# Optimization experiments

Hardware: AMD Instinct MI355X
Metric: run time of the kernel (lower is better)

Reference implementation:

```python
import math
import jax
import jax.numpy as jnp
from jax import lax
import numpy as np

B, T, S, C, E = 16, 1024, 2048, 256, 256
STRIDE, MAX_SAMPLES, SIGMA, RAND_START = 20, 20, 3.0, 0


def setup_inputs():
    key = jax.random.key(0)
    ks = jax.random.split(key, 6)
    return {
        "x": jax.random.normal(ks[0], (B, T, C), jnp.float32),
        "target_embedding": jax.random.normal(ks[1], (B, T, E), jnp.float32),
        # scale keys so pre-softmax scores are O(1..10) like a trained model
        "enc_keys": jax.random.normal(ks[2], (B, E, S), jnp.float32) * 0.05,
        "enc_values": jax.random.normal(ks[3], (B, S, E), jnp.float32),
        "W_in": jax.random.normal(ks[4], (E, C), jnp.float32) * math.sqrt(1.0 / C),
        "b_in": jnp.zeros((E,), jnp.float32),
        "W_out": jax.random.normal(ks[5], (C, E), jnp.float32) * math.sqrt(1.0 / E),
        "b_out": jnp.zeros((C,), jnp.float32),
    }


def _get_matrix(attn, sim_vec, stride, start):
    # attn: [B,T,S], sim_vec: [B,S,E]
    nrm = sim_vec / jnp.linalg.norm(sim_vec, axis=2, keepdims=True)
    attn_avg = jnp.mean(attn, axis=1)[..., None]          # [B,S,1]
    ns = nrm[:, start::stride, :]                          # [B,N,E]
    aa = attn_avg[:, start::stride, :]                     # [B,N,1]
    sim = jnp.einsum('bne,bme->bnm', ns, ns)               # cosine similarity
    qual = aa @ jnp.swapaxes(aa, 1, 2)                     # quality outer product
    return qual * sim                                      # DPP kernel L [B,N,N]


def _bfgm(L, max_samples):
    # Vectorized faithful version of the greedy Cholesky DPP MAP loop.
    Bv, N, _ = L.shape
    bidx = jnp.arange(Bv)
    D0 = jnp.diagonal(L, axis1=1, axis2=2)                 # [B,N]
    mask0 = jnp.ones((Bv, N), L.dtype)
    J0 = jnp.argmax(jnp.log(D0 * mask0), axis=1)
    mask0 = mask0.at[bidx, J0].set(0.0)
    C0 = jnp.zeros((Bv, N, max_samples), L.dtype)          # col 0 stays zero (as in torch)

    def step(carry, t):
        Cm, D, J, mask = carry
        Lj = L[bidx, J, :]                                 # [B,N] = L[b, J[b], i]
        cj = Cm[bidx, J, :]                                # [B,K]
        cdot = jnp.einsum('bnk,bk->bn', Cm, cj)            # <c_i, c_j>
        dj = D[bidx, J][:, None]
        e = (Lj - cdot) / dj * mask                        # zero at already-selected
        Cm = Cm.at[:, :, t].set(e)
        D = D - e * e
        J = jnp.argmax(jnp.log(D * mask), axis=1)
        mask = mask.at[bidx, J].set(0.0)
        return (Cm, D, J, mask), J

    (_, _, _, _), Js = lax.scan(step, (C0, D0, J0, mask0), jnp.arange(1, max_samples))
    all_J = jnp.concatenate([J0[None, :], Js], axis=0).T   # [B,max_samples]
    return jnp.sort(all_J, axis=1)                         # = nonzero(1-mask) order


def _create_gm(mu, sigma, length):
    pos = jnp.arange(length, dtype=jnp.float32)            # [S]
    z = pos[None, None, :] - mu[:, :, None].astype(jnp.float32)
    g = jnp.exp(-(z * z) / (2.0 * sigma * sigma)) / (math.sqrt(2.0 * math.pi) * sigma)
    return jnp.sum(g, axis=1)                              # [B,S]


def _forward(x, target_embedding, enc_keys, enc_values, W_in, b_in, W_out, b_out):
    residual = x
    h = (jnp.einsum('btc,ec->bte', x, W_in) + b_in + target_embedding) * math.sqrt(0.5)
    scores = jnp.einsum('bte,bes->bts', h, enc_keys)       # [B,T,S]
    attn = jax.nn.softmax(scores, axis=-1)
    # DPP auxiliary KL loss (training path, encoder_padding_mask=None); the
    # kernel / greedy selection / target distribution carry no gradient.
    L = _get_matrix(lax.stop_gradient(attn), lax.stop_gradient(enc_values), STRIDE, RAND_START)
    mu = _bfgm(L, MAX_SAMPLES)
    dist = jax.nn.softmax(_create_gm(mu, SIGMA, scores.shape[2]), axis=1)
    x_mean = jnp.mean(attn, axis=1)                        # [B,S]
    kl = jnp.sum(x_mean * (jnp.log(x_mean) - dist))        # KLDivLoss(input=dist, target=x_mean, sum)
    out = jnp.einsum('bts,bse->bte', attn, enc_values)
    s = enc_values.shape[1]
    out = out * (s * math.sqrt(1.0 / s))                   # = sqrt(s)
    out = (jnp.einsum('bte,ce->btc', out, W_out) + b_out + residual) * math.sqrt(0.5)
    return out, attn, -kl


def reference(x, target_embedding, enc_keys, enc_values, W_in, b_in, W_out, b_out):
    return _forward(x, target_embedding, enc_keys, enc_values, W_in, b_in, W_out, b_out)
```

## Files before the change

### kernel.cpp

```cpp
#include <hip/hip_runtime.h>
#include <math.h>

#define BB 16
#define TT 1024
#define SS 2048
#define CC 256
#define EE 256
#define NSUB 103
#define MAXS 20
#define STRIDE_ 20
#define XCH 32

static constexpr float RSQRT2  = 0.70710678118654752440f;
static constexpr float SQRT_S  = 45.25483399593904f;
static constexpr float GNORM   = 0.13298076013381093f;
static constexpr float INV2S2  = 0.055555555555555555f;

typedef __attribute__((ext_vector_type(8))) __bf16 bf16x8;
typedef __attribute__((ext_vector_type(4))) float  f32x4;

__device__ __forceinline__ float wave_sum(float v) {
    #pragma unroll
    for (int o = 32; o; o >>= 1) v += __shfl_down(v, o);
    return v;
}
__device__ __forceinline__ float wave_max(float v) {
    #pragma unroll
    for (int o = 32; o; o >>= 1) v = fmaxf(v, __shfl_down(v, o));
    return v;
}
__device__ __forceinline__ unsigned short f2bf(float f) {
    unsigned int u = __float_as_uint(f);
    u = (u + 0x7FFFu + ((u >> 16) & 1u)) >> 16;
    return (unsigned short)u;
}
__device__ __forceinline__ float bf2f(unsigned short s) {
    return __uint_as_float(((unsigned int)s) << 16);
}

#define GLD_LDS16(g, l) __builtin_amdgcn_global_load_lds(                      \
    (const __attribute__((address_space(1))) void*)(g),                        \
    (__attribute__((address_space(3))) void*)(l), 16, 0, 0)

__global__ __launch_bounds__(256) void k_cast3(
    const float* __restrict__ a,  unsigned short* __restrict__ oa, int na,
    const float* __restrict__ b2, unsigned short* __restrict__ ob, int nb,
    const float* __restrict__ c2, unsigned short* __restrict__ oc, int nc)
{
    int i = blockIdx.x * 256 + threadIdx.x;
    const float* in; unsigned short* out;
    if (i < na)                { in = a;  out = oa; }
    else if (i < na + nb)      { in = b2; out = ob; i -= na; }
    else if (i < na + nb + nc) { in = c2; out = oc; i -= na + nb; }
    else return;
    const float4 v = reinterpret_cast<const float4*>(in)[i];
    union { unsigned short u[4]; unsigned long long v8; } pk;
    pk.u[0] = f2bf(v.x); pk.u[1] = f2bf(v.y);
    pk.u[2] = f2bf(v.z); pk.u[3] = f2bf(v.w);
    reinterpret_cast<unsigned long long*>(out)[i] = pk.v8;
}

__global__ __launch_bounds__(256) void k_transpose2(
    const float* __restrict__ keys, unsigned short* __restrict__ keysT,
    const float* __restrict__ vals, unsigned short* __restrict__ valsT)
{
    __shared__ float t[64][65];
    const int id = blockIdx.x;
    const float* in; unsigned short* out;
    int R, Cc, bx, by, b;
    if (id < 2048) {
        in = keys; out = keysT; R = EE; Cc = SS;
        bx = id & 3; by = (id >> 2) & 31; b = id >> 7;
    } else {
        const int id2 = id - 2048;
        in = vals; out = valsT; R = SS; Cc = EE;
        bx = id2 & 31; by = (id2 >> 5) & 3; b = id2 >> 7;
    }
    const int r0 = bx * 64, c0 = by * 64;
    const float* ip = in + (size_t)b * R * Cc;
    unsigned short* op = out + (size_t)b * R * Cc;
    const int tx = threadIdx.x & 63, ty = threadIdx.x >> 6;
    #pragma unroll
    for (int i = 0; i < 16; ++i)
        t[ty + 4 * i][tx] = ip[(size_t)(r0 + ty + 4 * i) * Cc + c0 + tx];
    __syncthreads();
    #pragma unroll
    for (int i = 0; i < 16; ++i)
        op[(size_t)(c0 + ty + 4 * i) * R + r0 + tx] = f2bf(t[tx][ty + 4 * i]);
}

template<int BM, int BN, int MODE>
__global__ __launch_bounds__(256) void k_gemm(
    const unsigned short* __restrict__ Abase,
    const unsigned short* __restrict__ Btbase,
    const float* __restrict__ bias, const float* __restrict__ add,
    float* __restrict__ Obase, unsigned short* __restrict__ Obbase,
    int M, int Nn, int K, float scale)
{
    constexpr int BK = 64;
    constexpr int AR = BM / 32;
    constexpr int BR = BN / 32;
    constexpr int WM = BM / 2, WN = BN / 2;
    constexpr int MI = WM / 16, NJ = WN / 16;

    __shared__ unsigned short As[BM * BK];
    __shared__ unsigned short Bs[BN * BK];

    const int nwg = gridDim.x * gridDim.y * gridDim.z;
    int l = blockIdx.x + gridDim.x * (blockIdx.y + gridDim.y * blockIdx.z);
    if ((nwg & 7) == 0) l = (l & 7) * (nwg >> 3) + (l >> 3);
    const int bx = l % gridDim.x; l /= gridDim.x;
    const int by = l % gridDim.y;
    const int b  = l / gridDim.y;

    const int m0 = bx * BM;
    const int n0 = by * BN;
    const unsigned short* A  = Abase  + (size_t)b * M  * K;
    const unsigned short* Bt = Btbase + (size_t)b * Nn * K;

    const int tid  = threadIdx.x;
    const int w    = tid >> 6;
    const int lane = tid & 63;
    const int wm   = w & 1, wn = w >> 1;

    const int sr  = tid >> 3;
    const int skb = ((tid & 7) << 4) ^ ((sr & 7) << 4);
    const unsigned short* ga[AR];
    const unsigned short* gb[BR];
    #pragma unroll
    for (int p = 0; p < AR; ++p)
        ga[p] = A + (size_t)(m0 + p * 32 + sr) * K + (skb >> 1);
    #pragma unroll
    for (int p = 0; p < BR; ++p)
        gb[p] = Bt + (size_t)(n0 + p * 32 + sr) * K + (skb >> 1);

    const int fr = lane & 15;
    const int qb = (lane >> 4) << 4;

    f32x4 acc[MI][NJ];
    #pragma unroll
    for (int i = 0; i < MI; ++i)
        #pragma unroll
        for (int j = 0; j < NJ; ++j)
            acc[i][j] = (f32x4){0.f, 0.f, 0.f, 0.f};

    for (int k0 = 0; k0 < K; k0 += BK) {
        #pragma unroll
        for (int p = 0; p < AR; ++p) GLD_LDS16(ga[p], As + p * 2048 + w * 512);
        #pragma unroll
        for (int p = 0; p < BR; ++p) GLD_LDS16(gb[p], Bs + p * 2048 + w * 512);
        #pragma unroll
        for (int p = 0; p < AR; ++p) ga[p] += BK;
        #pragma unroll
        for (int p = 0; p < BR; ++p) gb[p] += BK;
        __syncthreads();
        #pragma unroll
        for (int c = 0; c < 2; ++c) {
            bf16x8 af[MI], bf[NJ];
            #pragma unroll
            for (int i = 0; i < MI; ++i) {
                const int row = wm * WM + i * 16 + fr;
                const int byt = row * 128 + ((c * 64 + qb) ^ ((row & 7) << 4));
                af[i] = *reinterpret_cast<const bf16x8*>(
                            reinterpret_cast<const char*>(As) + byt);
            }
            #pragma unroll
            for (int j = 0; j < NJ; ++j) {
                const int row = wn * WN + j * 16 + fr;
                const int byt = row * 128 + ((c * 64 + qb) ^ ((row & 7) << 4));
                bf[j] = *reinterpret_cast<const bf16x8*>(
                            reinterpret_cast<const char*>(Bs) + byt);
            }
            #pragma unroll
            for (int i = 0; i < MI; ++i)
                #pragma unroll
                for (int j = 0; j < NJ; ++j)
                    acc[i][j] = __builtin_amdgcn_mfma_f32_16x16x32_bf16(af[i], bf[j], acc[i][j], 0, 0, 0);
        }
        __syncthreads();
    }

    float* Of = (MODE == 0 || MODE == 1) ? Obase + (size_t)b * M * Nn : nullptr;
    unsigned short* Ob = (MODE == 2 || MODE == 3) ? Obbase + (size_t)b * M * Nn : nullptr;
    const int rb = (lane >> 4) * 4;
    #pragma unroll
    for (int i = 0; i < MI; ++i)
        #pragma unroll
        for (int j = 0; j < NJ; ++j) {
            const int n = n0 + wn * WN + j * 16 + fr;
            #pragma unroll
            for (int r2 = 0; r2 < 4; ++r2) {
                const int m = m0 + wm * WM + i * 16 + rb + r2;
                const size_t idx = (size_t)m * Nn + n;
                if (MODE == 0) {
                    Of[idx] = acc[i][j][r2] * scale;
                } else if (MODE == 1) {
                    Of[idx] = (acc[i][j][r2] + bias[n] + add[idx]) * RSQRT2;
                } else if (MODE == 2) {
                    Ob[idx] = f2bf((acc[i][j][r2] + bias[n] + add[idx]) * RSQRT2);
                } else {
                    Ob[idx] = f2bf(acc[i][j][r2] * scale);
                }
            }
        }
}

__global__ __launch_bounds__(256) void k_softmax(float* __restrict__ attn,
                                                 unsigned short* __restrict__ attnb)
{
    const int row  = blockIdx.x * 4 + (threadIdx.x >> 6);
    const int lane = threadIdx.x & 63;
    float* p = attn + (size_t)row * SS;
    unsigned short* pb = attnb + (size_t)row * SS;

    float v[32];
    #pragma unroll
    for (int s = 0; s < 4; ++s) {
        union { unsigned short u[8]; uint4 q; } ld;
        ld.q = *reinterpret_cast<const uint4*>(&pb[s * 512 + lane * 8]);
        #pragma unroll
        for (int i = 0; i < 8; ++i) v[s * 8 + i] = bf2f(ld.u[i]);
    }
    float mx = v[0];
    #pragma unroll
    for (int i = 1; i < 32; ++i) mx = fmaxf(mx, v[i]);
    #pragma unroll
    for (int o = 32; o; o >>= 1) mx = fmaxf(mx, __shfl_xor(mx, o));
    float s = 0.f;
    #pragma unroll
    for (int i = 0; i < 32; ++i) { v[i] = expf(v[i] - mx); s += v[i]; }
    #pragma unroll
    for (int o = 32; o; o >>= 1) s += __shfl_xor(s, o);
    const float inv = 1.0f / s;
    #pragma unroll
    for (int seg = 0; seg < 4; ++seg) {
        float4 o0, o1;
        o0.x = v[seg * 8 + 0] * inv; o0.y = v[seg * 8 + 1] * inv;
        o0.z = v[seg * 8 + 2] * inv; o0.w = v[seg * 8 + 3] * inv;
        o1.x = v[seg * 8 + 4] * inv; o1.y = v[seg * 8 + 5] * inv;
        o1.z = v[seg * 8 + 6] * inv; o1.w = v[seg * 8 + 7] * inv;
        *reinterpret_cast<float4*>(&p[seg * 512 + lane * 8])     = o0;
        *reinterpret_cast<float4*>(&p[seg * 512 + lane * 8 + 4]) = o1;
        union { unsigned short u[8]; uint4 q; } pk;
        pk.u[0] = f2bf(o0.x); pk.u[1] = f2bf(o0.y); pk.u[2] = f2bf(o0.z); pk.u[3] = f2bf(o0.w);
        pk.u[4] = f2bf(o1.x); pk.u[5] = f2bf(o1.y); pk.u[6] = f2bf(o1.z); pk.u[7] = f2bf(o1.w);
        *reinterpret_cast<uint4*>(&pb[seg * 512 + lane * 8]) = pk.q;
    }
}

__global__ __launch_bounds__(256) void k_xmean_part(const unsigned short* __restrict__ attnb,
                                                    float* __restrict__ part)
{
    const int c = blockIdx.x, b = blockIdx.y;
    const unsigned short* p = attnb + ((size_t)b * TT + (size_t)c * (TT / XCH)) * SS
                              + threadIdx.x * 8;
    float acc[8] = {0.f, 0.f, 0.f, 0.f, 0.f, 0.f, 0.f, 0.f};
    #pragma unroll 8
    for (int t = 0; t < TT / XCH; ++t) {
        union { unsigned short u[8]; uint4 v4; } ld;
        ld.v4 = *reinterpret_cast<const uint4*>(p + (size_t)t * SS);
        #pragma unroll
        for (int i = 0; i < 8; ++i) acc[i] += bf2f(ld.u[i]);
    }
    float* o = part + ((size_t)b * XCH + c) * SS + threadIdx.x * 8;
    #pragma unroll
    for (int i = 0; i < 8; ++i) o[i] = acc[i];
}

__global__ __launch_bounds__(256) void k_ns(const float* __restrict__ ev,
                                            const float* __restrict__ part,
                                            float* __restrict__ ns, float* __restrict__ aa,
                                            float* __restrict__ klp)
{
    const int n = blockIdx.x, b = blockIdx.y;
    const int tid = threadIdx.x;
    if (n == 0 && b == 0 && tid == 0) klp[0] = 0.0f;
    const float* rowp = ev + ((size_t)b * SS + (size_t)n * STRIDE_) * EE;
    const float v = rowp[tid];
    __shared__ float w[4];
    float r = wave_sum(v * v);
    if ((tid & 63) == 0) w[tid >> 6] = r;
    float pv = (tid < XCH) ? part[((size_t)b * XCH + tid) * SS + n * STRIDE_] : 0.f;
    float psum = wave_sum(pv);
    __syncthreads();
    const float nrm = sqrtf(w[0] + w[1] + w[2] + w[3]);
    ns[((size_t)b * NSUB + n) * EE + tid] = v / nrm;
    if (tid == 0) aa[b * NSUB + n] = psum * (1.0f / TT);
}

__global__ __launch_bounds__(128) void k_L(const float* __restrict__ ns,
                                           const float* __restrict__ aa,
                                           float* __restrict__ Lm)
{
    const int i = blockIdx.x, b = blockIdx.y;
    const int tid = threadIdx.x;
    __shared__ float nsi[EE];
    nsi[tid]       = ns[((size_t)b * NSUB + i) * EE + tid];
    nsi[tid + 128] = ns[((size_t)b * NSUB + i) * EE + tid + 128];
    __syncthreads();
    const float ai = aa[b * NSUB + i];
    for (int j = tid; j < NSUB; j += 128) {
        const float* rj = ns + ((size_t)b * NSUB + j) * EE;
        float d = 0.f;
        #pragma unroll 4
        for (int e = 0; e < EE; ++e) d += nsi[e] * rj[e];
        Lm[((size_t)b * NSUB + i) * NSUB + j] = d * ai * aa[b * NSUB + j];
    }
}

__global__ __launch_bounds__(256) void k_bfgm_kl(const float* __restrict__ Lm,
                                                 const float* __restrict__ part,
                                                 float* __restrict__ outkl)
{
    const int b = blockIdx.x;
    const int tid = threadIdx.x;
    const float* L = Lm + (size_t)b * NSUB * NSUB;
    __shared__ float D[128], mask[128], Cm[128 * 21], cj[MAXS], musS[MAXS];
    __shared__ float rv[4];
    __shared__ int   ri[4];
    __shared__ int   Jsh;
    __shared__ float w[4];
    const bool half = tid < 128;
    const bool act  = tid < NSUB;
    if (half) {
        D[tid]    = act ? L[(size_t)tid * NSUB + tid] : 0.0f;
        mask[tid] = act ? 1.0f : 0.0f;
        #pragma unroll
        for (int k = 0; k < MAXS; ++k) Cm[tid * 21 + k] = 0.0f;
    }
    __syncthreads();

    auto argmax_step = [&](int t) {
        float key = act ? logf(D[tid] * mask[tid]) : -INFINITY;
        if (isnan(key)) key = INFINITY;
        float v = key; int idx = tid;
        #pragma unroll
        for (int o = 32; o; o >>= 1) {
            float ov = __shfl_down(v, o); int oi = __shfl_down(idx, o);
            if (ov > v || (ov == v && oi < idx)) { v = ov; idx = oi; }
        }
        if ((tid & 63) == 0) { rv[tid >> 6] = v; ri[tid >> 6] = idx; }
        __syncthreads();
        if (tid == 0) {
            float bv = rv[0]; int bi = ri[0];
            #pragma unroll
            for (int q2 = 1; q2 < 4; ++q2)
                if (rv[q2] > bv || (rv[q2] == bv && ri[q2] < bi)) { bv = rv[q2]; bi = ri[q2]; }
            Jsh = bi; mask[bi] = 0.0f; musS[t] = (float)bi;
        }
        __syncthreads();
    };

    argmax_step(0);
    for (int t = 1; t < MAXS; ++t) {
        if (tid < MAXS) cj[tid] = Cm[Jsh * 21 + tid];
        __syncthreads();
        const int J = Jsh;
        const float dj = D[J];
        float e = 0.0f;
        if (act) {
            const float Ljn = L[(size_t)J * NSUB + tid];
            float cd = 0.f;
            #pragma unroll
            for (int k = 0; k < MAXS; ++k) cd += Cm[tid * 21 + k] * cj[k];
            e = (Ljn - cd) / dj * mask[tid];
        }
        if (half) { Cm[tid * 21 + t] = e; D[tid] -= e * e; }
        __syncthreads();
        argmax_step(t);
    }

    float xm[8];
    #pragma unroll
    for (int i = 0; i < 8; ++i) {
        float s = 0.f;
        #pragma unroll 8
        for (int c2 = 0; c2 < XCH; ++c2)
            s += part[((size_t)b * XCH + c2) * SS + tid + (i << 8)];
        xm[i] = s * (1.0f / TT);
    }
    float g[8];
    float mx = -INFINITY;
    #pragma unroll
    for (int i = 0; i < 8; ++i) {
        const float s = (float)(tid + (i << 8));
        float acc = 0.f;
        #pragma unroll
        for (int m = 0; m < MAXS; ++m) { const float z = s - musS[m]; acc += expf(-(z * z) * INV2S2); }
        g[i] = acc * GNORM;
        mx = fmaxf(mx, g[i]);
    }
    float wm = wave_max(mx);
    if ((tid & 63) == 0) w[tid >> 6] = wm;
    __syncthreads();
    const float m = fmaxf(fmaxf(w[0], w[1]), fmaxf(w[2], w[3]));
    float sum = 0.f;
    #pragma unroll
    for (int i = 0; i < 8; ++i) { g[i] = expf(g[i] - m); sum += g[i]; }
    __syncthreads();
    float wsv = wave_sum(sum);
    if ((tid & 63) == 0) w[tid >> 6] = wsv;
    __syncthreads();
    const float inv = 1.0f / (w[0] + w[1] + w[2] + w[3]);
    float acc2 = 0.f;
    #pragma unroll
    for (int i = 0; i < 8; ++i)
        acc2 += xm[i] * (logf(xm[i]) - g[i] * inv);
    __syncthreads();
    float wp = wave_sum(acc2);
    if ((tid & 63) == 0) w[tid >> 6] = wp;
    __syncthreads();
    if (tid == 0) atomicAdd(outkl, -(w[0] + w[1] + w[2] + w[3]));
}

extern "C" void kernel_launch(void* const* d_in, const int* in_sizes, int n_in,
                              void* d_out, int out_size, void* d_ws, size_t ws_size,
                              hipStream_t stream)
{
    const float* x     = (const float*)d_in[0];
    const float* te    = (const float*)d_in[1];
    const float* keys  = (const float*)d_in[2];
    const float* vals  = (const float*)d_in[3];
    const float* W_in  = (const float*)d_in[4];
    const float* b_in  = (const float*)d_in[5];
    const float* W_out = (const float*)d_in[6];
    const float* b_out = (const float*)d_in[7];

    float* outp = (float*)d_out;
    float* attn = outp + (size_t)BB * TT * CC;
    float* klp  = attn + (size_t)BB * TT * SS;

    unsigned short* X       = (unsigned short*)d_ws;
    unsigned short* x_bf    = X;
    unsigned short* Win_bf  = x_bf   + (size_t)BB * TT * CC;
    unsigned short* Wout_bf = Win_bf + (size_t)EE * CC;
    unsigned short* h_bf    = Wout_bf+ (size_t)CC * EE;
    unsigned short* keysT   = h_bf   + (size_t)BB * TT * EE;
    unsigned short* valsT   = keysT  + (size_t)BB * SS * EE;
    unsigned short* attnb   = valsT  + (size_t)BB * EE * SS;
    unsigned short* mid_bf  = attnb  + (size_t)BB * TT * SS;
    float* fws   = (float*)(mid_bf + (size_t)BB * TT * EE + 8);
    float* part  = fws;
    float* ns    = part  + (size_t)BB * XCH * SS;
    float* aa    = ns    + (size_t)BB * NSUB * EE;
    float* Lm    = aa    + (size_t)BB * NSUB;

    {
        const int na = BB * TT * CC / 4, nb = EE * CC / 4, nc = CC * EE / 4;
        const int blocks = (na + nb + nc + 255) / 256;
        k_cast3<<<blocks, 256, 0, stream>>>(x, x_bf, na, W_in, Win_bf, nb, W_out, Wout_bf, nc);
    }
    k_gemm<64, 64, 2><<<dim3(256, 4, 1), 256, 0, stream>>>(
        x_bf, Win_bf, b_in, te, nullptr, h_bf, BB * TT, CC, CC, 1.0f);
    k_transpose2<<<4096, 256, 0, stream>>>(keys, keysT, vals, valsT);
    k_gemm<128, 128, 3><<<dim3(8, 16, BB), 256, 0, stream>>>(
        h_bf, keysT, nullptr, nullptr, nullptr, attnb, TT, SS, EE, 1.0f);
    k_softmax<<<BB * TT / 4, 256, 0, stream>>>(attn, attnb);
    k_xmean_part<<<dim3(XCH, BB), 256, 0, stream>>>(attnb, part);
    k_ns<<<dim3(NSUB, BB), 256, 0, stream>>>(vals, part, ns, aa, klp);
    k_L<<<dim3(NSUB, BB), 128, 0, stream>>>(ns, aa, Lm);
    k_bfgm_kl<<<BB, 256, 0, stream>>>(Lm, part, klp);
    k_gemm<64, 128, 3><<<dim3(16, 2, BB), 256, 0, stream>>>(
        attnb, valsT, nullptr, nullptr, nullptr, mid_bf, TT, EE, SS, SQRT_S);
    k_gemm<64, 64, 1><<<dim3(256, 4, 1), 256, 0, stream>>>(
        mid_bf, Wout_bf, b_out, x, outp, nullptr, BB * TT, CC, CC, 1.0f);
}
```

Measured before the change: 460.1 us.

## Fuse normalization into L kernel and run greedy DPP loop in one wave

Removes the separate k_ns kernel by computing row norms and attention averages inside the L-matrix kernel, which reads enc_values rows directly with float4 loads. The greedy Cholesky DPP selection is rewritten to run within a single 64-lane wave, two items per lane, using shuffles for the argmax instead of block-wide syncthreads. The goal is to cut one launch and the many barriers in the sequential 20-step loop. In exchange, each j row's norm is recomputed redundantly across blocks, and correctness now depends on single-wave LDS visibility through __threadfence_block.

```diff
diff --git a/kernel.cpp b/kernel.cpp
--- a/kernel.cpp
+++ b/kernel.cpp
@@ -249,9 +249,11 @@
 }
 
 __global__ __launch_bounds__(256) void k_xmean_part(const unsigned short* __restrict__ attnb,
-                                                    float* __restrict__ part)
+                                                    float* __restrict__ part,
+                                                    float* __restrict__ klp)
 {
     const int c = blockIdx.x, b = blockIdx.y;
+    if (c == 0 && b == 0 && threadIdx.x == 0) klp[0] = 0.0f;
     const unsigned short* p = attnb + ((size_t)b * TT + (size_t)c * (TT / XCH)) * SS
                               + threadIdx.x * 8;
     float acc[8] = {0.f, 0.f, 0.f, 0.f, 0.f, 0.f, 0.f, 0.f};
@@ -267,44 +269,41 @@
     for (int i = 0; i < 8; ++i) o[i] = acc[i];
 }
 
-__global__ __launch_bounds__(256) void k_ns(const float* __restrict__ ev,
-                                            const float* __restrict__ part,
-                                            float* __restrict__ ns, float* __restrict__ aa,
-                                            float* __restrict__ klp)
-{
-    const int n = blockIdx.x, b = blockIdx.y;
-    const int tid = threadIdx.x;
-    if (n == 0 && b == 0 && tid == 0) klp[0] = 0.0f;
-    const float* rowp = ev + ((size_t)b * SS + (size_t)n * STRIDE_) * EE;
-    const float v = rowp[tid];
-    __shared__ float w[4];
-    float r = wave_sum(v * v);
-    if ((tid & 63) == 0) w[tid >> 6] = r;
-    float pv = (tid < XCH) ? part[((size_t)b * XCH + tid) * SS + n * STRIDE_] : 0.f;
-    float psum = wave_sum(pv);
-    __syncthreads();
-    const float nrm = sqrtf(w[0] + w[1] + w[2] + w[3]);
-    ns[((size_t)b * NSUB + n) * EE + tid] = v / nrm;
-    if (tid == 0) aa[b * NSUB + n] = psum * (1.0f / TT);
-}
-
-__global__ __launch_bounds__(128) void k_L(const float* __restrict__ ns,
-                                           const float* __restrict__ aa,
-                                           float* __restrict__ Lm)
+__global__ __launch_bounds__(128) void k_L_direct(const float* __restrict__ ev,
+                                                  const float* __restrict__ part,
+                                                  float* __restrict__ Lm)
 {
     const int i = blockIdx.x, b = blockIdx.y;
     const int tid = threadIdx.x;
-    __shared__ float nsi[EE];
-    nsi[tid]       = ns[((size_t)b * NSUB + i) * EE + tid];
-    nsi[tid + 128] = ns[((size_t)b * NSUB + i) * EE + tid + 128];
-    __syncthreads();
-    const float ai = aa[b * NSUB + i];
+    __shared__ float evi[EE];
+    __shared__ float aaS[NSUB];
+    __shared__ float w[2];
+    const float* rowi = ev + ((size_t)b * SS + (size_t)i * STRIDE_) * EE;
+    const float v0 = rowi[tid], v1 = rowi[tid + 128];
+    evi[tid] = v0; evi[tid + 128] = v1;
+    const float r = wave_sum(v0 * v0 + v1 * v1);
+    if ((tid & 63) == 0) w[tid >> 6] = r;
+    if (tid < NSUB) {
+        float s = 0.f;
+        #pragma unroll 8
+        for (int c2 = 0; c2 < XCH; ++c2)
+            s += part[((size_t)b * XCH + c2) * SS + tid * STRIDE_];
+        aaS[tid] = s * (1.0f / TT);
+    }
+    __syncthreads();
+    const float nrmi = sqrtf(w[0] + w[1]);
+    const float ai = aaS[i];
     for (int j = tid; j < NSUB; j += 128) {
-        const float* rj = ns + ((size_t)b * NSUB + j) * EE;
-        float d = 0.f;
+        const float* rj = ev + ((size_t)b * SS + (size_t)j * STRIDE_) * EE;
+        float d = 0.f, n2 = 0.f;
         #pragma unroll 4
-        for (int e = 0; e < EE; ++e) d += nsi[e] * rj[e];
-        Lm[((size_t)b * NSUB + i) * NSUB + j] = d * ai * aa[b * NSUB + j];
+        for (int e = 0; e < EE; e += 4) {
+            const float4 a4 = *reinterpret_cast<const float4*>(&evi[e]);
+            const float4 b4 = *reinterpret_cast<const float4*>(&rj[e]);
+            d  += a4.x * b4.x + a4.y * b4.y + a4.z * b4.z + a4.w * b4.w;
+            n2 += b4.x * b4.x + b4.y * b4.y + b4.z * b4.z + b4.w * b4.w;
+        }
+        Lm[((size_t)b * NSUB + i) * NSUB + j] = d * ai * aaS[j] / (nrmi * sqrtf(n2));
     }
 }
 
@@ -315,60 +314,9 @@
     const int b = blockIdx.x;
     const int tid = threadIdx.x;
     const float* L = Lm + (size_t)b * NSUB * NSUB;
-    __shared__ float D[128], mask[128], Cm[128 * 21], cj[MAXS], musS[MAXS];
-    __shared__ float rv[4];
-    __shared__ int   ri[4];
-    __shared__ int   Jsh;
+    __shared__ float CmL[128 * 21];
+    __shared__ float musS[MAXS];
     __shared__ float w[4];
-    const bool half = tid < 128;
-    const bool act  = tid < NSUB;
-    if (half) {
-        D[tid]    = act ? L[(size_t)tid * NSUB + tid] : 0.0f;
-        mask[tid] = act ? 1.0f : 0.0f;
-        #pragma unroll
-        for (int k = 0; k < MAXS; ++k) Cm[tid * 21 + k] = 0.0f;
-    }
-    __syncthreads();
-
-    auto argmax_step = [&](int t) {
-        float key = act ? logf(D[tid] * mask[tid]) : -INFINITY;
-        if (isnan(key)) key = INFINITY;
-        float v = key; int idx = tid;
-        #pragma unroll
-        for (int o = 32; o; o >>= 1) {
-            float ov = __shfl_down(v, o); int oi = __shfl_down(idx, o);
-            if (ov > v || (ov == v && oi < idx)) { v = ov; idx = oi; }
-        }
-        if ((tid & 63) == 0) { rv[tid >> 6] = v; ri[tid >> 6] = idx; }
-        __syncthreads();
-        if (tid == 0) {
-            float bv = rv[0]; int bi = ri[0];
-            #pragma unroll
-            for (int q2 = 1; q2 < 4; ++q2)
-                if (rv[q2] > bv || (rv[q2] == bv && ri[q2] < bi)) { bv = rv[q2]; bi = ri[q2]; }
-            Jsh = bi; mask[bi] = 0.0f; musS[t] = (float)bi;
-        }
-        __syncthreads();
-    };
-
-    argmax_step(0);
-    for (int t = 1; t < MAXS; ++t) {
-        if (tid < MAXS) cj[tid] = Cm[Jsh * 21 + tid];
-        __syncthreads();
-        const int J = Jsh;
-        const float dj = D[J];
-        float e = 0.0f;
-        if (act) {
-            const float Ljn = L[(size_t)J * NSUB + tid];
-            float cd = 0.f;
-            #pragma unroll
-            for (int k = 0; k < MAXS; ++k) cd += Cm[tid * 21 + k] * cj[k];
-            e = (Ljn - cd) / dj * mask[tid];
-        }
-        if (half) { Cm[tid * 21 + t] = e; D[tid] -= e * e; }
-        __syncthreads();
-        argmax_step(t);
-    }
 
     float xm[8];
     #pragma unroll
@@ -379,6 +327,53 @@
             s += part[((size_t)b * XCH + c2) * SS + tid + (i << 8)];
         xm[i] = s * (1.0f / TT);
     }
+
+    if (tid < 64) {
+        const int i0 = tid, i1 = tid + 64;
+        const bool a1 = (i1 < NSUB);
+        float D0 = L[(size_t)i0 * NSUB + i0];
+        float D1 = a1 ? L[(size_t)i1 * NSUB + i1] : 0.0f;
+        float m0 = 1.0f, m1 = a1 ? 1.0f : 0.0f;
+        #pragma unroll
+        for (int k = 0; k < MAXS; ++k) { CmL[i0 * 21 + k] = 0.0f; CmL[i1 * 21 + k] = 0.0f; }
+        #pragma unroll 1
+        for (int t = 0; t < MAXS; ++t) {
+            float k0 = logf(D0 * m0); if (isnan(k0)) k0 = INFINITY;
+            float k1 = a1 ? logf(D1 * m1) : -INFINITY; if (isnan(k1)) k1 = INFINITY;
+            float v = k0; int idx = i0;
+            if (k1 > v) { v = k1; idx = i1; }
+            #pragma unroll
+            for (int o = 32; o; o >>= 1) {
+                const float ov = __shfl_down(v, o);
+                const int   oi = __shfl_down(idx, o);
+                if (ov > v || (ov == v && oi < idx)) { v = ov; idx = oi; }
+            }
+            const int J = __shfl(idx, 0);
+            if (J == i0) m0 = 0.0f;
+            if (J == i1) m1 = 0.0f;
+            if (tid == 0) musS[t] = (float)J;
+            if (t == MAXS - 1) break;
+            const float Dsel = (J >= 64) ? D1 : D0;
+            const float dj = __shfl(Dsel, J & 63);
+            const float Lj0 = L[(size_t)J * NSUB + i0];
+            const float Lj1 = a1 ? L[(size_t)J * NSUB + i1] : 0.0f;
+            float cd0 = 0.0f, cd1 = 0.0f;
+            for (int k = 1; k <= t; ++k) {
+                const float cjk = CmL[J * 21 + k];
+                cd0 += CmL[i0 * 21 + k] * cjk;
+                cd1 += CmL[i1 * 21 + k] * cjk;
+            }
+            const float e0 = (Lj0 - cd0) / dj * m0;
+            const float e1 = a1 ? (Lj1 - cd1) / dj * m1 : 0.0f;
+            CmL[i0 * 21 + t + 1] = e0;
+            CmL[i1 * 21 + t + 1] = e1;
+            __threadfence_block();
+            D0 -= e0 * e0;
+            D1 -= e1 * e1;
+        }
+    }
+    __syncthreads();
+
     float g[8];
     float mx = -INFINITY;
     #pragma unroll
@@ -441,9 +436,7 @@
     unsigned short* mid_bf  = attnb  + (size_t)BB * TT * SS;
     float* fws   = (float*)(mid_bf + (size_t)BB * TT * EE + 8);
     float* part  = fws;
-    float* ns    = part  + (size_t)BB * XCH * SS;
-    float* aa    = ns    + (size_t)BB * NSUB * EE;
-    float* Lm    = aa    + (size_t)BB * NSUB;
+    float* Lm    = part  + (size_t)BB * XCH * SS;
 
     {
         const int na = BB * TT * CC / 4, nb = EE * CC / 4, nc = CC * EE / 4;
@@ -456,9 +449,8 @@
     k_gemm<128, 128, 3><<<dim3(8, 16, BB), 256, 0, stream>>>(
         h_bf, keysT, nullptr, nullptr, nullptr, attnb, TT, SS, EE, 1.0f);
     k_softmax<<<BB * TT / 4, 256, 0, stream>>>(attn, attnb);
-    k_xmean_part<<<dim3(XCH, BB), 256, 0, stream>>>(attnb, part);
-    k_ns<<<dim3(NSUB, BB), 256, 0, stream>>>(vals, part, ns, aa, klp);
-    k_L<<<dim3(NSUB, BB), 128, 0, stream>>>(ns, aa, Lm);
+    k_xmean_part<<<dim3(XCH, BB), 256, 0, stream>>>(attnb, part, klp);
+    k_L_direct<<<dim3(NSUB, BB), 128, 0, stream>>>(vals, part, Lm);
     k_bfgm_kl<<<BB, 256, 0, stream>>>(Lm, part, klp);
     k_gemm<64, 128, 3><<<dim3(16, 2, BB), 256, 0, stream>>>(
         attnb, valsT, nullptr, nullptr, nullptr, mid_bf, TT, EE, SS, SQRT_S);
```

After: 443.1 us. -3.7%, faster.
